# Performance work log

Measured on AMD Instinct MI355X. Metric: run time of the kernel, lower is better.

The kernel has to match this reference:

```python
import jax, jax.numpy as jnp
import numpy as np

EPS = 1e-6
H, DH = 8, 128

def rms_norm(x):
    return x * jax.lax.rsqrt(jnp.mean(jnp.square(x), axis=-1, keepdims=True) + EPS)

def l2norm(x):
    return x * jax.lax.rsqrt(jnp.sum(jnp.square(x), axis=-1, keepdims=True) + EPS)

def gated_deltanet(x, state, wq, wk, wv, wb, wg, wo):
    B, T, D = x.shape
    # projections; silu + per-head L2 norm on q,k (DeltaNet convention), silu on v
    q = l2norm(jax.nn.silu(x @ wq).reshape(B, T, H, DH))
    k = l2norm(jax.nn.silu(x @ wk).reshape(B, T, H, DH))
    v = jax.nn.silu(x @ wv).reshape(B, T, H, DH)
    beta = jax.nn.sigmoid(x @ wb)   # [B,T,H] learning-rate gate
    alpha = jax.nn.sigmoid(x @ wg)  # [B,T,H] decay gate

    def step(S, inp):
        qt, kt, vt, bt, at = inp  # [B,H,DH], [B,H,DH], [B,H,DH], [B,H], [B,H]
        S = at[..., None, None] * S                      # gated decay
        pred = jnp.einsum('bhk,bhkv->bhv', kt, S)        # S^T k
        dv = bt[..., None] * (vt - pred)                 # delta-rule update
        S = S + kt[..., None] * dv[:, :, None, :]        # rank-1 write k (x) dv
        ot = jnp.einsum('bhk,bhkv->bhv', qt, S)
        return S, ot

    tm = lambda a: jnp.moveaxis(a, 1, 0)  # time-major
    S_final, o = jax.lax.scan(step, state, (tm(q), tm(k), tm(v), tm(beta), tm(alpha)))
    o = jnp.moveaxis(o, 0, 1).reshape(B, T, H * DH)
    return o @ wo, S_final

def swiglu(x, w_gate, w_up, w_down):
    return (jax.nn.silu(x @ w_gate) * (x @ w_up)) @ w_down

def setup_inputs() -> dict:
    key = jax.random.key(0)
    ks = jax.random.split(key, 12)
    B, T, D, F = 2, 2048, 1024, 4096
    s = 1.0 / np.sqrt(D)
    inp = {
        'x': jax.random.normal(ks[0], (B, T, D), jnp.float32),
        'recurrent_state': jnp.zeros((B, H, DH, DH), jnp.float32),
        'wq': jax.random.normal(ks[1], (D, H * DH), jnp.float32) * s,
        'wk': jax.random.normal(ks[2], (D, H * DH), jnp.float32) * s,
        'wv': jax.random.normal(ks[3], (D, H * DH), jnp.float32) * s,
        'wb': jax.random.normal(ks[4], (D, H), jnp.float32) * s,
        'wg': jax.random.normal(ks[5], (D, H), jnp.float32) * s,
        'wo': jax.random.normal(ks[6], (H * DH, D), jnp.float32) * s,
        'w_gate': jax.random.normal(ks[7], (D, F), jnp.float32) * s,
        'w_up': jax.random.normal(ks[8], (D, F), jnp.float32) * s,
        'w_down': jax.random.normal(ks[9], (F, D), jnp.float32) * (1.0 / np.sqrt(F)),
    }
    return inp

def reference(x, recurrent_state, wq, wk, wv, wb, wg, wo, w_gate, w_up, w_down):
    attn_out, new_state = gated_deltanet(rms_norm(x), recurrent_state, wq, wk, wv, wb, wg, wo)
    x = x + attn_out
    x = x + swiglu(rms_norm(x), w_gate, w_up, w_down)
    return x, new_state
```

## Files before the change

### kernel.cpp

```cpp
#include <hip/hip_runtime.h>
#include <hip/hip_bf16.h>
#include <math.h>

#define BSZ 2
#define TLEN 2048
#define DDIM 1024
#define FDIM 4096
#define HHEADS 8
#define DHEAD 128
#define NC 32
#define CS 64

typedef __bf16 bf16x8 __attribute__((ext_vector_type(8)));
typedef float f32x4 __attribute__((ext_vector_type(4)));

__device__ __forceinline__ float silu_f(float x) {
    return x / (1.0f + expf(-x));
}

__device__ __forceinline__ void load_lds16(const void* g, void* l) {
    __builtin_amdgcn_global_load_lds(
        (const __attribute__((address_space(1))) void*)g,
        (__attribute__((address_space(3))) void*)l, 16, 0, 0);
}

__device__ __forceinline__ unsigned short bf16_bits(float f) {
    __hip_bfloat16 h = __float2bfloat16(f);
    return *reinterpret_cast<unsigned short*>(&h);
}

__device__ __forceinline__ float bfbits2f(unsigned short u) {
    union { unsigned int i; float f; } c;
    c.i = ((unsigned int)u) << 16;
    return c.f;
}

__device__ __forceinline__ uint4 pack8_bf16(const float* f) {
    union { unsigned short u[8]; uint4 v; } r;
#pragma unroll
    for (int i = 0; i < 8; ++i) r.u[i] = bf16_bits(f[i]);
    return r.v;
}

struct alignas(8) bh4 { __hip_bfloat16 a, b, c, d; };

__global__ __launch_bounds__(256) void rmsnorm_k(const float* __restrict__ in,
                                                 __hip_bfloat16* __restrict__ out) {
    const long row = blockIdx.x;
    const int tid = threadIdx.x;
    const float4 x = *(const float4*)(in + row * DDIM + tid * 4);
    float ss = x.x * x.x + x.y * x.y + x.z * x.z + x.w * x.w;
    ss += __shfl_xor(ss, 1);
    ss += __shfl_xor(ss, 2);
    ss += __shfl_xor(ss, 4);
    ss += __shfl_xor(ss, 8);
    ss += __shfl_xor(ss, 16);
    ss += __shfl_xor(ss, 32);
    __shared__ float wsum[4];
    if ((tid & 63) == 0) wsum[tid >> 6] = ss;
    __syncthreads();
    const float tot = wsum[0] + wsum[1] + wsum[2] + wsum[3];
    const float sc = rsqrtf(tot * (1.0f / (float)DDIM) + 1e-6f);
    bh4 y;
    y.a = __float2bfloat16(x.x * sc);
    y.b = __float2bfloat16(x.y * sc);
    y.c = __float2bfloat16(x.z * sc);
    y.d = __float2bfloat16(x.w * sc);
    *(bh4*)(out + row * DDIM + tid * 4) = y;
}

__global__ __launch_bounds__(256) void transpose_cvt(const float* __restrict__ W,
                                                     __hip_bfloat16* __restrict__ Wt,
                                                     int K, int N) {
    __shared__ float t[32][33];
    const int n0 = blockIdx.x * 32, k0 = blockIdx.y * 32;
    const int tx = threadIdx.x & 31, ty = threadIdx.x >> 5;
#pragma unroll
    for (int i = 0; i < 4; ++i)
        t[ty * 4 + i][tx] = W[(long)(k0 + ty * 4 + i) * N + n0 + tx];
    __syncthreads();
#pragma unroll
    for (int i = 0; i < 4; ++i)
        Wt[(long)(n0 + ty * 4 + i) * K + k0 + tx] = __float2bfloat16(t[tx][ty * 4 + i]);
}

template <int MODE>
__global__ __launch_bounds__(256) void gemm_n64(const __hip_bfloat16* __restrict__ A,
                                                const __hip_bfloat16* __restrict__ Bt,
                                                const float* __restrict__ resid,
                                                void* __restrict__ Cout,
                                                int M, int N, int K) {
    __shared__ __align__(16) short As[4 * 128 * 32];
    __shared__ __align__(16) short Bs[4 * 64 * 32];
    const int tid = threadIdx.x;
    const int w = tid >> 6, l = tid & 63;
    const int m0 = blockIdx.y * 128, n0 = blockIdx.x * 64;
    const int srow = (w << 4) + (l >> 2);
    const int skcol = (l & 3) * 8;
    const int wr = w >> 1, wc = w & 1;
    const int fr = l & 15;
    const int fkB = (l >> 4) * 16;

    f32x4 acc[4][2];
#pragma unroll
    for (int m = 0; m < 4; ++m)
#pragma unroll
        for (int n = 0; n < 2; ++n) acc[m][n] = (f32x4)0.0f;

    const __hip_bfloat16* Abase = A + (long)m0 * K + skcol;
    const __hip_bfloat16* Bbase = Bt + (long)n0 * K + skcol;

    for (int k0 = 0; k0 < K; k0 += 128) {
#pragma unroll
        for (int p = 0; p < 4; ++p) {
#pragma unroll
            for (int j = 0; j < 2; ++j)
                load_lds16(Abase + (long)(srow + j * 64) * K + k0 + p * 32,
                           (char*)As + p * 8192 + w * 1024 + j * 4096);
            load_lds16(Bbase + (long)srow * K + k0 + p * 32,
                       (char*)Bs + p * 4096 + w * 1024);
        }
        __syncthreads();
#pragma unroll
        for (int p = 0; p < 4; ++p) {
            bf16x8 av[4], bv[2];
#pragma unroll
            for (int m = 0; m < 4; ++m)
                av[m] = *(const bf16x8*)((char*)As + p * 8192 + (wr * 64 + m * 16 + fr) * 64 + fkB);
#pragma unroll
            for (int n = 0; n < 2; ++n)
                bv[n] = *(const bf16x8*)((char*)Bs + p * 4096 + (wc * 32 + n * 16 + fr) * 64 + fkB);
#pragma unroll
            for (int m = 0; m < 4; ++m)
#pragma unroll
                for (int n = 0; n < 2; ++n)
                    acc[m][n] = __builtin_amdgcn_mfma_f32_16x16x32_bf16(av[m], bv[n], acc[m][n], 0, 0, 0);
        }
        __syncthreads();
    }

    const int r0 = (l >> 4) * 4;
    const int cc = l & 15;
#pragma unroll
    for (int m = 0; m < 4; ++m) {
#pragma unroll
        for (int r = 0; r < 4; ++r) {
            const long row = m0 + wr * 64 + m * 16 + r0 + r;
            const long colb = n0 + wc * 32 + cc;
            if (MODE == 2) {
                __hip_bfloat16* cb = (__hip_bfloat16*)Cout + row * N + colb;
#pragma unroll
                for (int n = 0; n < 2; ++n)
                    cb[n * 16] = __float2bfloat16(acc[m][n][r]);
            } else {
                float* cp = (float*)Cout + row * N + colb;
                const float* rp = resid + row * N + colb;
#pragma unroll
                for (int n = 0; n < 2; ++n)
                    cp[n * 16] = acc[m][n][r] + rp[n * 16];
            }
        }
    }
}

__global__ __launch_bounds__(256) void gemm_gateup_bf16(const __hip_bfloat16* __restrict__ A,
                                                        const __hip_bfloat16* __restrict__ Bg,
                                                        const __hip_bfloat16* __restrict__ Bu,
                                                        __hip_bfloat16* __restrict__ Hb,
                                                        int M, int N, int K) {
    __shared__ __align__(16) short As[2 * 128 * 32];
    __shared__ __align__(16) short Bgs[2 * 64 * 32];
    __shared__ __align__(16) short Bus[2 * 64 * 32];
    const int tid = threadIdx.x;
    const int w = tid >> 6, l = tid & 63;
    const int m0 = blockIdx.y * 128, n0 = blockIdx.x * 64;
    const int srow = (w << 4) + (l >> 2);
    const int skcol = (l & 3) * 8;
    const int wr = w >> 1, wc = w & 1;
    const int fr = l & 15;
    const int fkB = (l >> 4) * 16;

    f32x4 accg[4][2], accu[4][2];
#pragma unroll
    for (int m = 0; m < 4; ++m)
#pragma unroll
        for (int n = 0; n < 2; ++n) { accg[m][n] = (f32x4)0.0f; accu[m][n] = (f32x4)0.0f; }

    const __hip_bfloat16* Abase = A + (long)m0 * K + skcol;
    const __hip_bfloat16* Bgb = Bg + (long)n0 * K + skcol;
    const __hip_bfloat16* Bub = Bu + (long)n0 * K + skcol;

    for (int k0 = 0; k0 < K; k0 += 64) {
#pragma unroll
        for (int p = 0; p < 2; ++p) {
#pragma unroll
            for (int j = 0; j < 2; ++j)
                load_lds16(Abase + (long)(srow + j * 64) * K + k0 + p * 32,
                           (char*)As + p * 8192 + w * 1024 + j * 4096);
            load_lds16(Bgb + (long)srow * K + k0 + p * 32, (char*)Bgs + p * 4096 + w * 1024);
            load_lds16(Bub + (long)srow * K + k0 + p * 32, (char*)Bus + p * 4096 + w * 1024);
        }
        __syncthreads();
#pragma unroll
        for (int p = 0; p < 2; ++p) {
            bf16x8 av[4], bgv[2], buv[2];
#pragma unroll
            for (int m = 0; m < 4; ++m)
                av[m] = *(const bf16x8*)((char*)As + p * 8192 + (wr * 64 + m * 16 + fr) * 64 + fkB);
#pragma unroll
            for (int n = 0; n < 2; ++n) {
                bgv[n] = *(const bf16x8*)((char*)Bgs + p * 4096 + (wc * 32 + n * 16 + fr) * 64 + fkB);
                buv[n] = *(const bf16x8*)((char*)Bus + p * 4096 + (wc * 32 + n * 16 + fr) * 64 + fkB);
            }
#pragma unroll
            for (int m = 0; m < 4; ++m)
#pragma unroll
                for (int n = 0; n < 2; ++n) {
                    accg[m][n] = __builtin_amdgcn_mfma_f32_16x16x32_bf16(av[m], bgv[n], accg[m][n], 0, 0, 0);
                    accu[m][n] = __builtin_amdgcn_mfma_f32_16x16x32_bf16(av[m], buv[n], accu[m][n], 0, 0, 0);
                }
        }
        __syncthreads();
    }

    const int r0 = (l >> 4) * 4;
    const int cc = l & 15;
#pragma unroll
    for (int m = 0; m < 4; ++m) {
#pragma unroll
        for (int r = 0; r < 4; ++r) {
            const long row = m0 + wr * 64 + m * 16 + r0 + r;
            __hip_bfloat16* hp = Hb + row * N + n0 + wc * 32 + cc;
#pragma unroll
            for (int n = 0; n < 2; ++n)
                hp[n * 16] = __float2bfloat16(silu_f(accg[m][n][r]) * accu[m][n][r]);
        }
    }
}

__global__ __launch_bounds__(64) void ba_kernel(const float* __restrict__ x,
                                                const float* __restrict__ wb,
                                                const float* __restrict__ wg,
                                                float* __restrict__ beta,
                                                float* __restrict__ alpha) {
    __shared__ float xs[DDIM];
    const long row = blockIdx.x;
    const int tid = threadIdx.x;
    float ss = 0.0f;
#pragma unroll
    for (int j = 0; j < 4; ++j) {
        const int fi = tid + j * 64;
        const float4 v = *(const float4*)(x + row * DDIM + fi * 4);
        *(float4*)&xs[fi * 4] = v;
        ss += v.x * v.x + v.y * v.y + v.z * v.z + v.w * v.w;
    }
    ss += __shfl_xor(ss, 1);
    ss += __shfl_xor(ss, 2);
    ss += __shfl_xor(ss, 4);
    ss += __shfl_xor(ss, 8);
    ss += __shfl_xor(ss, 16);
    ss += __shfl_xor(ss, 32);
    __syncthreads();
    const int o = tid >> 2;
    const int p = tid & 3;
    const float* wbase = (o < 8) ? (wb + o) : (wg + (o - 8));
    const float* wr = wbase + (long)(p * 256) * HHEADS;
    const float* xr = xs + p * 256;
    float acc = 0.0f;
#pragma unroll 8
    for (int i = 0; i < 256; ++i)
        acc = fmaf(xr[i], wr[(long)i * HHEADS], acc);
    acc += __shfl_xor(acc, 1);
    acc += __shfl_xor(acc, 2);
    if (p == 0) {
        const float sc = rsqrtf(ss * (1.0f / (float)DDIM) + 1e-6f);
        const float val = 1.0f / (1.0f + expf(-acc * sc));
        if (o < 8) beta[row * HHEADS + o] = val;
        else       alpha[row * HHEADS + (o - 8)] = val;
    }
}

__global__ __launch_bounds__(64) void postqkv(__hip_bfloat16* __restrict__ q,
                                              __hip_bfloat16* __restrict__ k,
                                              __hip_bfloat16* __restrict__ v) {
    const long r = blockIdx.x;
    const int tid = threadIdx.x;
    {
        unsigned int* qp = (unsigned int*)(q + r * DHEAD + tid * 2);
        const unsigned int wbits = *qp;
        float y0 = silu_f(bfbits2f(wbits & 0xffff));
        float y1 = silu_f(bfbits2f(wbits >> 16));
        float ss = y0 * y0 + y1 * y1;
        ss += __shfl_xor(ss, 1);  ss += __shfl_xor(ss, 2);
        ss += __shfl_xor(ss, 4);  ss += __shfl_xor(ss, 8);
        ss += __shfl_xor(ss, 16); ss += __shfl_xor(ss, 32);
        const float sc = rsqrtf(ss + 1e-6f);
        *qp = (unsigned int)bf16_bits(y0 * sc) | ((unsigned int)bf16_bits(y1 * sc) << 16);
    }
    {
        unsigned int* kp = (unsigned int*)(k + r * DHEAD + tid * 2);
        const unsigned int wbits = *kp;
        float y0 = silu_f(bfbits2f(wbits & 0xffff));
        float y1 = silu_f(bfbits2f(wbits >> 16));
        float ss = y0 * y0 + y1 * y1;
        ss += __shfl_xor(ss, 1);  ss += __shfl_xor(ss, 2);
        ss += __shfl_xor(ss, 4);  ss += __shfl_xor(ss, 8);
        ss += __shfl_xor(ss, 16); ss += __shfl_xor(ss, 32);
        const float sc = rsqrtf(ss + 1e-6f);
        *kp = (unsigned int)bf16_bits(y0 * sc) | ((unsigned int)bf16_bits(y1 * sc) << 16);
    }
    {
        unsigned int* vp = (unsigned int*)(v + r * DHEAD + tid * 2);
        const unsigned int wbits = *vp;
        *vp = (unsigned int)bf16_bits(silu_f(bfbits2f(wbits & 0xffff)))
            | ((unsigned int)bf16_bits(silu_f(bfbits2f(wbits >> 16))) << 16);
    }
}


__global__ __launch_bounds__(256) void chunk_prep(
    const __hip_bfloat16* __restrict__ kb, const __hip_bfloat16* __restrict__ qb,
    const __hip_bfloat16* __restrict__ vb, const float* __restrict__ betab,
    const float* __restrict__ alphab, float* __restrict__ Gcum,
    __hip_bfloat16* __restrict__ Rg, __hip_bfloat16* __restrict__ Ktg,
    __hip_bfloat16* __restrict__ dvX, __hip_bfloat16* __restrict__ Mmat)
{
    const int bh = blockIdx.x >> 5;
    const int c  = blockIdx.x & 31;
    const int b = bh >> 3, h = bh & 7;
    const int tid = threadIdx.x;
    const int w = tid >> 6, l = tid & 63;
    const int fr = l & 15;
    const int fk8 = (l >> 4) * 8;
    const int fr4 = (l >> 4) * 4;

    __shared__ __align__(16) char smem[64512];
    __hip_bfloat16* tA  = (__hip_bfloat16*)(smem);
    __hip_bfloat16* Tm  = (__hip_bfloat16*)(smem + 17408);
    __hip_bfloat16* Xr  = (__hip_bfloat16*)(smem + 26624);
    __hip_bfloat16* Xt  = (__hip_bfloat16*)(smem + 35840);
    __hip_bfloat16* bvT = (__hip_bfloat16*)(smem + 26624);
    __hip_bfloat16* tB  = (__hip_bfloat16*)(smem + 45056);
    __hip_bfloat16* KtS = (__hip_bfloat16*)(smem + 45056);
    float* sa  = (float*)(smem + 63488);
    float* sb_ = sa + 64;
    float* sG  = sb_ + 64;
    float* swB = sG + 64;

    const long row0 = (long)b * TLEN + (long)c * CS;
    const long chnk = (long)bh * NC + c;

    if (tid < 64) {
        sa[tid]  = alphab[(row0 + tid) * HHEADS + h];
        sb_[tid] = betab[(row0 + tid) * HHEADS + h];
    }
    {
        const int r = tid >> 2;
        const int d0 = (tid & 3) * 32;
        const uint4* kp = (const uint4*)(kb + (row0 + r) * DDIM + h * DHEAD + d0);
        const uint4* qp = (const uint4*)(qb + (row0 + r) * DDIM + h * DHEAD + d0);
#pragma unroll
        for (int i = 0; i < 4; ++i) {
            *(uint4*)&tA[r * 136 + d0 + i * 8] = kp[i];
            *(uint4*)&tB[r * 136 + d0 + i * 8] = qp[i];
        }
    }
    __syncthreads();
    if (tid < 64) {
        float lv = logf(sa[tid]);
#pragma unroll
        for (int off = 1; off < 64; off <<= 1) {
            const float o = __shfl_up(lv, off, 64);
            if (tid >= off) lv += o;
        }
        sG[tid] = lv;
        Gcum[chnk * CS + tid] = lv;
        swB[tid] = sb_[tid] * expf(lv);
    }
    __syncthreads();

    f32x4 accW[4], accM[4];
#pragma unroll
    for (int n = 0; n < 4; ++n) { accW[n] = (f32x4)0.0f; accM[n] = (f32x4)0.0f; }
#pragma unroll
    for (int ks = 0; ks < 4; ++ks) {
        const bf16x8 aW = *(const bf16x8*)&tA[(w * 16 + fr) * 136 + ks * 32 + fk8];
        const bf16x8 aM = *(const bf16x8*)&tB[(w * 16 + fr) * 136 + ks * 32 + fk8];
#pragma unroll
        for (int n = 0; n < 4; ++n) {
            const bf16x8 bfr = *(const bf16x8*)&tA[(n * 16 + fr) * 136 + ks * 32 + fk8];
            accW[n] = __builtin_amdgcn_mfma_f32_16x16x32_bf16(aW, bfr, accW[n], 0, 0, 0);
            accM[n] = __builtin_amdgcn_mfma_f32_16x16x32_bf16(aM, bfr, accM[n], 0, 0, 0);
        }
    }
#pragma unroll
    for (int n = 0; n < 4; ++n) {
        const int s = n * 16 + fr;
        const float Gs = sG[s];
#pragma unroll
        for (int r = 0; r < 4; ++r) {
            const int t = w * 16 + fr4 + r;
            const float ratio = (s <= t) ? expf(sG[t] - Gs) : 0.0f;
            Mmat[(chnk * CS + t) * CS + s] = __float2bfloat16(ratio * accM[n][r]);
            const float xv = (s < t) ? -(sb_[t] * ratio * accW[n][r]) : 0.0f;
            const __hip_bfloat16 xb = __float2bfloat16(xv);
            Xr[t * 72 + s] = xb;
            Xt[s * 72 + t] = xb;
            Tm[t * 72 + s] = __float2bfloat16((s == t) ? 1.0f : 0.0f);
        }
    }
    __syncthreads();

    {
        const int kk = tid >> 1;
        const int t0 = (tid & 1) * 32;
        __hip_bfloat16* kp = Ktg + (chnk * DHEAD + kk) * CS + t0;
        float f[8], fs[8];
#pragma unroll
        for (int i = 0; i < 4; ++i) {
#pragma unroll
            for (int j2 = 0; j2 < 8; ++j2) {
                const int t = t0 + i * 8 + j2;
                f[j2] = __bfloat162float(tA[t * 136 + kk]);
                fs[j2] = f[j2] * swB[t];
            }
            *(uint4*)(kp + i * 8) = pack8_bf16(f);
            *(uint4*)&KtS[kk * 72 + t0 + i * 8] = pack8_bf16(fs);
        }
    }
    __syncthreads();

    for (int rnd = 0; rnd < 6; ++rnd) {
        f32x4 aT[4], aXr2[4], aXt2[4];
#pragma unroll
        for (int n = 0; n < 4; ++n) { aT[n] = (f32x4)0.0f; aXr2[n] = (f32x4)0.0f; aXt2[n] = (f32x4)0.0f; }
#pragma unroll
        for (int ks = 0; ks < 2; ++ks) {
            const bf16x8 fT  = *(const bf16x8*)&Tm[(w * 16 + fr) * 72 + ks * 32 + fk8];
            const bf16x8 fXr = *(const bf16x8*)&Xr[(w * 16 + fr) * 72 + ks * 32 + fk8];
            const bf16x8 fXt = *(const bf16x8*)&Xt[(w * 16 + fr) * 72 + ks * 32 + fk8];
#pragma unroll
            for (int n = 0; n < 4; ++n) {
                const bf16x8 bXt = *(const bf16x8*)&Xt[(n * 16 + fr) * 72 + ks * 32 + fk8];
                const bf16x8 bXr = *(const bf16x8*)&Xr[(n * 16 + fr) * 72 + ks * 32 + fk8];
                aT[n]   = __builtin_amdgcn_mfma_f32_16x16x32_bf16(fT,  bXt, aT[n], 0, 0, 0);
                aXr2[n] = __builtin_amdgcn_mfma_f32_16x16x32_bf16(fXr, bXt, aXr2[n], 0, 0, 0);
                aXt2[n] = __builtin_amdgcn_mfma_f32_16x16x32_bf16(fXt, bXr, aXt2[n], 0, 0, 0);
            }
        }
        float told[4][4];
#pragma unroll
        for (int n = 0; n < 4; ++n)
#pragma unroll
            for (int r = 0; r < 4; ++r)
                told[n][r] = __bfloat162float(Tm[(w * 16 + fr4 + r) * 72 + n * 16 + fr]);
        __syncthreads();
#pragma unroll
        for (int n = 0; n < 4; ++n) {
            const int col = n * 16 + fr;
#pragma unroll
            for (int r = 0; r < 4; ++r) {
                const int t = w * 16 + fr4 + r;
                Tm[t * 72 + col] = __float2bfloat16(aT[n][r] + told[n][r]);
                if (rnd < 5) {
                    Xr[t * 72 + col] = __float2bfloat16(aXr2[n][r]);
                    Xt[t * 72 + col] = __float2bfloat16(aXt2[n][r]);
                }
            }
        }
        __syncthreads();
    }

    {
        f32x4 aR[8];
#pragma unroll
        for (int n = 0; n < 8; ++n) aR[n] = (f32x4)0.0f;
#pragma unroll
        for (int ks = 0; ks < 2; ++ks) {
            const bf16x8 aTf = *(const bf16x8*)&Tm[(w * 16 + fr) * 72 + ks * 32 + fk8];
#pragma unroll
            for (int n = 0; n < 8; ++n) {
                const bf16x8 bK = *(const bf16x8*)&KtS[(n * 16 + fr) * 72 + ks * 32 + fk8];
                aR[n] = __builtin_amdgcn_mfma_f32_16x16x32_bf16(aTf, bK, aR[n], 0, 0, 0);
            }
        }
#pragma unroll
        for (int n = 0; n < 8; ++n)
#pragma unroll
            for (int r = 0; r < 4; ++r) {
                const int t = w * 16 + fr4 + r;
                Rg[(chnk * CS + t) * DHEAD + n * 16 + fr] = __float2bfloat16(-aR[n][r]);
            }
    }

    {
        const int r = tid >> 2, d0 = (tid & 3) * 32;
        const float br = sb_[r];
        const uint4* vp = (const uint4*)(vb + (row0 + r) * DDIM + h * DHEAD + d0);
#pragma unroll
        for (int i = 0; i < 4; ++i) {
            const uint4 vv = vp[i];
            const unsigned short* u = (const unsigned short*)&vv;
#pragma unroll
            for (int j2 = 0; j2 < 8; ++j2)
                bvT[(d0 + i * 8 + j2) * 72 + r] = __float2bfloat16(br * bfbits2f(u[j2]));
        }
    }
    __syncthreads();

    {
        f32x4 aD[8];
#pragma unroll
        for (int n = 0; n < 8; ++n) aD[n] = (f32x4)0.0f;
#pragma unroll
        for (int ks = 0; ks < 2; ++ks) {
            const bf16x8 aTf = *(const bf16x8*)&Tm[(w * 16 + fr) * 72 + ks * 32 + fk8];
#pragma unroll
            for (int n = 0; n < 8; ++n) {
                const bf16x8 bV = *(const bf16x8*)&bvT[(n * 16 + fr) * 72 + ks * 32 + fk8];
                aD[n] = __builtin_amdgcn_mfma_f32_16x16x32_bf16(aTf, bV, aD[n], 0, 0, 0);
            }
        }
#pragma unroll
        for (int n = 0; n < 8; ++n)
#pragma unroll
            for (int r = 0; r < 4; ++r) {
                const int t = w * 16 + fr4 + r;
                dvX[(chnk * CS + t) * DHEAD + n * 16 + fr] = __float2bfloat16(aD[n][r]);
            }
    }
}

#define SEQGV 8
#define SEQ_LDS_BYTES 78848

__global__ __launch_bounds__(256) void chunk_seq_mfma(
    const float* __restrict__ S0in, const float* __restrict__ Gcum,
    const __hip_bfloat16* __restrict__ Rg, const __hip_bfloat16* __restrict__ Ktg,
    __hip_bfloat16* __restrict__ dvX, __hip_bfloat16* __restrict__ Ssnap,
    float* __restrict__ Sout)
{
    const int bh = blockIdx.x & 15;
    const int g  = blockIdx.x >> 4;
    const int j0 = g * 16;
    const int tid = threadIdx.x;
    const int w = tid >> 6;
    const int l = tid & 63;
    const int fr = l & 15;
    const int fk8 = (l >> 4) * 8;
    const int rq = (l >> 4) * 4;

    __shared__ __align__(16) char smem[SEQ_LDS_BYTES];
    __hip_bfloat16* dvT = (__hip_bfloat16*)(smem + 71680);
    __hip_bfloat16* Stl = (__hip_bfloat16*)(smem + 73984);
    float* sG = (float*)(smem + 78336);

    f32x4 SM[2];
#pragma unroll
    for (int mj = 0; mj < 2; ++mj) {
#pragma unroll
        for (int r = 0; r < 4; ++r) {
            const int kk = w * 32 + mj * 16 + rq + r;
            const float v = S0in[((long)bh * 128 + kk) * 128 + j0 + fr];
            SM[mj][r] = v;
            Stl[fr * 136 + kk] = __float2bfloat16(v);
        }
    }

    uint4 rreg[4], kreg[4];
    float greg = 0.0f;

#define SEQ_STAGE_LOAD(c_) do {                                                   \
        const long cb_ = (long)bh * NC + (c_);                                    \
        _Pragma("unroll")                                                         \
        for (int i_ = 0; i_ < 4; ++i_) {                                          \
            const int ur_ = (tid << 2) + i_;                                      \
            rreg[i_] = *(const uint4*)(Rg + (cb_ * CS + (ur_ >> 4)) * DHEAD + ((ur_ & 15) << 3)); \
            kreg[i_] = *(const uint4*)(Ktg + (cb_ * DHEAD + (ur_ >> 3)) * CS + ((ur_ & 7) << 3)); \
        }                                                                         \
        if (tid < 64) greg = Gcum[cb_ * CS + tid];                                \
    } while (0)

#define SEQ_STAGE_WRITE(bufi_) do {                                               \
        __hip_bfloat16* rb_ = (__hip_bfloat16*)(smem + (bufi_) * 17408);          \
        __hip_bfloat16* kb2_ = (__hip_bfloat16*)(smem + 34816 + (bufi_) * 18432); \
        _Pragma("unroll")                                                         \
        for (int i_ = 0; i_ < 4; ++i_) {                                          \
            const int ur_ = (tid << 2) + i_;                                      \
            *(uint4*)(rb_ + (ur_ >> 4) * 136 + ((ur_ & 15) << 3)) = rreg[i_];     \
            *(uint4*)(kb2_ + (ur_ >> 3) * 72 + ((ur_ & 7) << 3)) = kreg[i_];      \
        }                                                                         \
        if (tid < 64) sG[(bufi_) * 64 + tid] = greg;                              \
    } while (0)

    SEQ_STAGE_LOAD(0);
    SEQ_STAGE_WRITE(0);
    __syncthreads();

    for (int c = 0; c < NC; ++c) {
        const int cur = c & 1;
        const long chnk = (long)bh * NC + c;
        const __hip_bfloat16* Rl = (const __hip_bfloat16*)(smem + cur * 17408);
        const __hip_bfloat16* Ktl = (const __hip_bfloat16*)(smem + 34816 + cur * 18432);
        const float g63 = sG[cur * 64 + 63];
        const float a63 = expf(g63);

        unsigned short d0r[4];
#pragma unroll
        for (int r = 0; r < 4; ++r) {
            const int t = w * 16 + rq + r;
            d0r[r] = *(const unsigned short*)(dvX + (chnk * CS + t) * DHEAD + j0 + fr);
        }

        if (c + 1 < NC) SEQ_STAGE_LOAD(c + 1);

        {
            const int j = tid >> 4, k0 = (tid & 15) * 8;
            const uint4 v = *(const uint4*)&Stl[j * 136 + k0];
            *(uint4*)(Ssnap + (chnk * 128 + j0 + j) * 128 + k0) = v;
        }

        f32x4 acc = (f32x4)0.0f;
#pragma unroll
        for (int ks = 0; ks < 4; ++ks) {
            const bf16x8 bfrag = *(const bf16x8*)&Stl[fr * 136 + ks * 32 + fk8];
            const bf16x8 afrag = *(const bf16x8*)&Rl[(w * 16 + fr) * 136 + ks * 32 + fk8];
            acc = __builtin_amdgcn_mfma_f32_16x16x32_bf16(afrag, bfrag, acc, 0, 0, 0);
        }
#pragma unroll
        for (int r = 0; r < 4; ++r) {
            const int t = w * 16 + rq + r;
            const float rk = expf(g63 - sG[cur * 64 + t]);
            const float dv = acc[r] + bfbits2f(d0r[r]);
            *(unsigned short*)(dvX + (chnk * CS + t) * DHEAD + j0 + fr) = bf16_bits(dv);
            dvT[fr * 72 + t] = __float2bfloat16(rk * dv);
        }

        if (c + 1 < NC) SEQ_STAGE_WRITE(cur ^ 1);
        __syncthreads();

#pragma unroll
        for (int mj = 0; mj < 2; ++mj) SM[mj] *= a63;
#pragma unroll
        for (int ks = 0; ks < 2; ++ks) {
            const bf16x8 bfrag = *(const bf16x8*)&dvT[fr * 72 + ks * 32 + fk8];
#pragma unroll
            for (int mj = 0; mj < 2; ++mj) {
                const bf16x8 afrag = *(const bf16x8*)&Ktl[(w * 32 + mj * 16 + fr) * 72 + ks * 32 + fk8];
                SM[mj] = __builtin_amdgcn_mfma_f32_16x16x32_bf16(afrag, bfrag, SM[mj], 0, 0, 0);
            }
        }
#pragma unroll
        for (int mj = 0; mj < 2; ++mj)
#pragma unroll
            for (int r = 0; r < 4; ++r) {
                const int kk = w * 32 + mj * 16 + rq + r;
                Stl[fr * 136 + kk] = __float2bfloat16(SM[mj][r]);
            }
        __syncthreads();
    }

#pragma unroll
    for (int mj = 0; mj < 2; ++mj)
#pragma unroll
        for (int r = 0; r < 4; ++r) {
            const int kk = w * 32 + mj * 16 + rq + r;
            Sout[((long)bh * 128 + kk) * 128 + j0 + fr] = SM[mj][r];
        }
#undef SEQ_STAGE_LOAD
#undef SEQ_STAGE_WRITE
}

__global__ __launch_bounds__(256) void chunk_out(
    const __hip_bfloat16* __restrict__ qb, const float* __restrict__ Gcum,
    const __hip_bfloat16* __restrict__ dvX, const __hip_bfloat16* __restrict__ Ssnap,
    const __hip_bfloat16* __restrict__ Mmat, __hip_bfloat16* __restrict__ ob)
{
    const int bh = blockIdx.x >> 5;
    const int c  = blockIdx.x & 31;
    const int b = bh >> 3, h = bh & 7;
    const int tid = threadIdx.x;
    const int w = tid >> 6, l = tid & 63;
    const int fr = l & 15;
    const int fk8 = (l >> 4) * 8;
    const int rq = (l >> 4) * 4;
    const long row0 = (long)b * TLEN + (long)c * CS;
    const long chnk = (long)bh * NC + c;

    __shared__ __align__(16) char smem[62464];
    __hip_bfloat16* Ssn = (__hip_bfloat16*)(smem);
    __hip_bfloat16* Ml  = (__hip_bfloat16*)(smem + 34816);
    __hip_bfloat16* dq  = (__hip_bfloat16*)(smem + 44032);

    {
        const int j = tid >> 1;
        const int d0 = (tid & 1) * 64;
        const uint4* sp = (const uint4*)(Ssnap + (chnk * 128 + j) * 128 + d0);
#pragma unroll
        for (int i = 0; i < 8; ++i)
            *(uint4*)&Ssn[j * 136 + d0 + i * 8] = sp[i];
    }
    {
        const int t = tid >> 2;
        const int s0 = (tid & 3) * 16;
        const uint4* mp = (const uint4*)(Mmat + (chnk * CS + t) * CS + s0);
        *(uint4*)&Ml[t * 72 + s0]     = mp[0];
        *(uint4*)&Ml[t * 72 + s0 + 8] = mp[1];
    }
    {
        const int t = tid >> 2, jb = (tid & 3) * 32;
        uint4 dvr[4];
#pragma unroll
        for (int i = 0; i < 4; ++i)
            dvr[i] = ((const uint4*)(dvX + (chnk * CS + t) * DHEAD + jb))[i];
        const unsigned short* u = (const unsigned short*)&dvr[0];
#pragma unroll
        for (int i = 0; i < 32; ++i)
            dq[(jb + i) * 72 + t] = *(const __hip_bfloat16*)&u[i];
    }
    __syncthreads();

    f32x4 acc[8];
#pragma unroll
    for (int n = 0; n < 8; ++n) acc[n] = (f32x4)0.0f;

#pragma unroll
    for (int ks = 0; ks < 2; ++ks) {
        const bf16x8 afrag = *(const bf16x8*)&Ml[(w * 16 + fr) * 72 + ks * 32 + fk8];
#pragma unroll
        for (int n = 0; n < 8; ++n) {
            const bf16x8 bfrag = *(const bf16x8*)&dq[(n * 16 + fr) * 72 + ks * 32 + fk8];
            acc[n] = __builtin_amdgcn_mfma_f32_16x16x32_bf16(afrag, bfrag, acc[n], 0, 0, 0);
        }
    }
    __syncthreads();

    {
        const int t = tid >> 2, d0 = (tid & 3) * 32;
        const float At = expf(Gcum[chnk * CS + t]);
        const uint4* qp = (const uint4*)(qb + (row0 + t) * DDIM + h * DHEAD + d0);
#pragma unroll
        for (int i = 0; i < 4; ++i) {
            const uint4 qv = qp[i];
            const unsigned short* u = (const unsigned short*)&qv;
            float f[8];
#pragma unroll
            for (int j = 0; j < 8; ++j) f[j] = At * bfbits2f(u[j]);
            *(uint4*)&dq[t * 136 + d0 + i * 8] = pack8_bf16(f);
        }
    }
    __syncthreads();

#pragma unroll
    for (int ks = 0; ks < 4; ++ks) {
        const bf16x8 afrag = *(const bf16x8*)&dq[(w * 16 + fr) * 136 + ks * 32 + fk8];
#pragma unroll
        for (int n = 0; n < 8; ++n) {
            const bf16x8 bfrag = *(const bf16x8*)&Ssn[(n * 16 + fr) * 136 + ks * 32 + fk8];
            acc[n] = __builtin_amdgcn_mfma_f32_16x16x32_bf16(afrag, bfrag, acc[n], 0, 0, 0);
        }
    }

#pragma unroll
    for (int r = 0; r < 4; ++r) {
        const int t = w * 16 + rq + r;
        __hip_bfloat16* op = ob + (row0 + t) * DDIM + h * DHEAD + fr;
#pragma unroll
        for (int n = 0; n < 8; ++n)
            op[n * 16] = __float2bfloat16(acc[n][r]);
    }
}

extern "C" void kernel_launch(void* const* d_in, const int* in_sizes, int n_in,
                              void* d_out, int out_size, void* d_ws, size_t ws_size,
                              hipStream_t stream) {
    const float* x     = (const float*)d_in[0];
    const float* S0    = (const float*)d_in[1];
    const float* wq    = (const float*)d_in[2];
    const float* wk    = (const float*)d_in[3];
    const float* wv    = (const float*)d_in[4];
    const float* wb    = (const float*)d_in[5];
    const float* wg    = (const float*)d_in[6];
    const float* wo    = (const float*)d_in[7];
    const float* wgate = (const float*)d_in[8];
    const float* wup   = (const float*)d_in[9];
    const float* wdown = (const float*)d_in[10];

    const int M = BSZ * TLEN;

    float* out  = (float*)d_out;
    float* Sout = out + (long)M * DDIM;

    char* w = (char*)d_ws;
    const size_t MB = 1u << 20;
    const size_t KB = 1u << 10;
    __hip_bfloat16* qbh   = (__hip_bfloat16*)(w + 0 * MB);
    __hip_bfloat16* kbh   = (__hip_bfloat16*)(w + 8 * MB);
    __hip_bfloat16* vbh   = (__hip_bfloat16*)(w + 16 * MB);
    float*          beta  = (float*)(w + 24 * MB);
    float*          alpha = (float*)(w + 24 * MB + 128 * KB);
    float*          Gcum  = (float*)(w + 24 * MB + 256 * KB);
    __hip_bfloat16* Mmat  = (__hip_bfloat16*)(w + 24 * MB + 512 * KB);
    __hip_bfloat16* dvX   = (__hip_bfloat16*)(w + 28 * MB + 512 * KB);
    __hip_bfloat16* Rg    = (__hip_bfloat16*)(w + 36 * MB + 512 * KB);
    __hip_bfloat16* xnb   = (__hip_bfloat16*)(w + 36 * MB + 512 * KB);
    __hip_bfloat16* Ktg   = (__hip_bfloat16*)(w + 44 * MB + 512 * KB);
    __hip_bfloat16* Ssnap = (__hip_bfloat16*)(w + 52 * MB + 512 * KB);
    __hip_bfloat16* wqt   = (__hip_bfloat16*)(w + 68 * MB + 512 * KB);
    __hip_bfloat16* wkt   = (__hip_bfloat16*)(w + 70 * MB + 512 * KB);
    __hip_bfloat16* wvt   = (__hip_bfloat16*)(w + 72 * MB + 512 * KB);
    __hip_bfloat16* wot   = (__hip_bfloat16*)(w + 74 * MB + 512 * KB);
    __hip_bfloat16* obufb = (__hip_bfloat16*)(w + 8 * MB);
    __hip_bfloat16* xn2b  = (__hip_bfloat16*)(w + 8 * MB);
    __hip_bfloat16* wdt   = (__hip_bfloat16*)(w + 16 * MB);
    __hip_bfloat16* wgt   = (__hip_bfloat16*)(w + 24 * MB + 512 * KB);
    __hip_bfloat16* wut   = (__hip_bfloat16*)(w + 32 * MB + 512 * KB);
    __hip_bfloat16* Hb    = (__hip_bfloat16*)(w + 40 * MB + 512 * KB);

    transpose_cvt<<<dim3(DDIM / 32, DDIM / 32), 256, 0, stream>>>(wq, wqt, DDIM, DDIM);
    transpose_cvt<<<dim3(DDIM / 32, DDIM / 32), 256, 0, stream>>>(wk, wkt, DDIM, DDIM);
    transpose_cvt<<<dim3(DDIM / 32, DDIM / 32), 256, 0, stream>>>(wv, wvt, DDIM, DDIM);
    transpose_cvt<<<dim3(DDIM / 32, DDIM / 32), 256, 0, stream>>>(wo, wot, DDIM, DDIM);

    rmsnorm_k<<<M, 256, 0, stream>>>(x, xnb);
    ba_kernel<<<M, 64, 0, stream>>>(x, wb, wg, beta, alpha);

    dim3 gP64(DDIM / 64, M / 128);
    gemm_n64<2><<<gP64, 256, 0, stream>>>(xnb, wqt, nullptr, qbh, M, DDIM, DDIM);
    gemm_n64<2><<<gP64, 256, 0, stream>>>(xnb, wkt, nullptr, kbh, M, DDIM, DDIM);
    gemm_n64<2><<<gP64, 256, 0, stream>>>(xnb, wvt, nullptr, vbh, M, DDIM, DDIM);
    postqkv<<<M * HHEADS, 64, 0, stream>>>(qbh, kbh, vbh);

    chunk_prep<<<16 * NC, 256, 0, stream>>>(kbh, qbh, vbh, beta, alpha, Gcum, Rg, Ktg, dvX, Mmat);
    chunk_seq_mfma<<<16 * SEQGV, 256, 0, stream>>>(S0, Gcum, Rg, Ktg, dvX, Ssnap, Sout);
    chunk_out<<<16 * NC, 256, 0, stream>>>(qbh, Gcum, dvX, Ssnap, Mmat, obufb);

    gemm_n64<1><<<gP64, 256, 0, stream>>>(obufb, wot, x, out, M, DDIM, DDIM);

    transpose_cvt<<<dim3(DDIM / 32, FDIM / 32), 256, 0, stream>>>(wdown, wdt, FDIM, DDIM);
    transpose_cvt<<<dim3(FDIM / 32, DDIM / 32), 256, 0, stream>>>(wgate, wgt, DDIM, FDIM);
    transpose_cvt<<<dim3(FDIM / 32, DDIM / 32), 256, 0, stream>>>(wup, wut, DDIM, FDIM);

    rmsnorm_k<<<M, 256, 0, stream>>>(out, xn2b);

    dim3 gGU(FDIM / 64, M / 128);
    gemm_gateup_bf16<<<gGU, 256, 0, stream>>>(xn2b, wgt, wut, Hb, M, FDIM, DDIM);

    gemm_n64<1><<<gP64, 256, 0, stream>>>(Hb, wdt, out, out, M, DDIM, FDIM);
}
```

Before: 365.0 us.

## Fuse RMSNorm into gate kernel, merge QKV GEMMs, widen gate-up GEMM blocks

The first RMSNorm is folded into ba_kernel, which now also writes the normalized bf16 activations, so one launch and one extra read of x go away. The three Q/K/V projection GEMMs become a single launch with N=3072, using a new MODE 3 epilogue that scatters each 1024-column slice into its own output buffer. This relies on wqt/wkt/wvt and qbh/kbh/vbh being laid out contiguously. The gate-up GEMM moves to 512 threads per block, with each warp covering 32 rows instead of 64, which lowers per-thread accumulator pressure and spreads tile loading across more warps.

```diff
diff --git a/kernel.cpp b/kernel.cpp
--- a/kernel.cpp
+++ b/kernel.cpp
@@ -152,6 +152,12 @@
 #pragma unroll
                 for (int n = 0; n < 2; ++n)
                     cb[n * 16] = __float2bfloat16(acc[m][n][r]);
+            } else if (MODE == 3) {
+                __hip_bfloat16* cb = (__hip_bfloat16*)Cout
+                    + (long)(n0 >> 10) * 4194304 + row * 1024 + (colb & 1023);
+#pragma unroll
+                for (int n = 0; n < 2; ++n)
+                    cb[n * 16] = __float2bfloat16(acc[m][n][r]);
             } else {
                 float* cp = (float*)Cout + row * N + colb;
                 const float* rp = resid + row * N + colb;
@@ -163,7 +169,7 @@
     }
 }
 
-__global__ __launch_bounds__(256) void gemm_gateup_bf16(const __hip_bfloat16* __restrict__ A,
+__global__ __launch_bounds__(512) void gemm_gateup_bf16(const __hip_bfloat16* __restrict__ A,
                                                         const __hip_bfloat16* __restrict__ Bg,
                                                         const __hip_bfloat16* __restrict__ Bu,
                                                         __hip_bfloat16* __restrict__ Hb,
@@ -180,9 +186,9 @@
     const int fr = l & 15;
     const int fkB = (l >> 4) * 16;
 
-    f32x4 accg[4][2], accu[4][2];
-#pragma unroll
-    for (int m = 0; m < 4; ++m)
+    f32x4 accg[2][2], accu[2][2];
+#pragma unroll
+    for (int m = 0; m < 2; ++m)
 #pragma unroll
         for (int n = 0; n < 2; ++n) { accg[m][n] = (f32x4)0.0f; accu[m][n] = (f32x4)0.0f; }
 
@@ -193,27 +199,29 @@
     for (int k0 = 0; k0 < K; k0 += 64) {
 #pragma unroll
         for (int p = 0; p < 2; ++p) {
-#pragma unroll
-            for (int j = 0; j < 2; ++j)
-                load_lds16(Abase + (long)(srow + j * 64) * K + k0 + p * 32,
-                           (char*)As + p * 8192 + w * 1024 + j * 4096);
-            load_lds16(Bgb + (long)srow * K + k0 + p * 32, (char*)Bgs + p * 4096 + w * 1024);
-            load_lds16(Bub + (long)srow * K + k0 + p * 32, (char*)Bus + p * 4096 + w * 1024);
+            load_lds16(Abase + (long)srow * K + k0 + p * 32,
+                       (char*)As + p * 8192 + w * 1024);
+            if (w < 4)
+                load_lds16(Bgb + (long)srow * K + k0 + p * 32,
+                           (char*)Bgs + p * 4096 + w * 1024);
+            else
+                load_lds16(Bub + (long)(srow - 64) * K + k0 + p * 32,
+                           (char*)Bus + p * 4096 + (w - 4) * 1024);
         }
         __syncthreads();
 #pragma unroll
         for (int p = 0; p < 2; ++p) {
-            bf16x8 av[4], bgv[2], buv[2];
-#pragma unroll
-            for (int m = 0; m < 4; ++m)
-                av[m] = *(const bf16x8*)((char*)As + p * 8192 + (wr * 64 + m * 16 + fr) * 64 + fkB);
+            bf16x8 av[2], bgv[2], buv[2];
+#pragma unroll
+            for (int m = 0; m < 2; ++m)
+                av[m] = *(const bf16x8*)((char*)As + p * 8192 + (wr * 32 + m * 16 + fr) * 64 + fkB);
 #pragma unroll
             for (int n = 0; n < 2; ++n) {
                 bgv[n] = *(const bf16x8*)((char*)Bgs + p * 4096 + (wc * 32 + n * 16 + fr) * 64 + fkB);
                 buv[n] = *(const bf16x8*)((char*)Bus + p * 4096 + (wc * 32 + n * 16 + fr) * 64 + fkB);
             }
 #pragma unroll
-            for (int m = 0; m < 4; ++m)
+            for (int m = 0; m < 2; ++m)
 #pragma unroll
                 for (int n = 0; n < 2; ++n) {
                     accg[m][n] = __builtin_amdgcn_mfma_f32_16x16x32_bf16(av[m], bgv[n], accg[m][n], 0, 0, 0);
@@ -226,10 +234,10 @@
     const int r0 = (l >> 4) * 4;
     const int cc = l & 15;
 #pragma unroll
-    for (int m = 0; m < 4; ++m) {
+    for (int m = 0; m < 2; ++m) {
 #pragma unroll
         for (int r = 0; r < 4; ++r) {
-            const long row = m0 + wr * 64 + m * 16 + r0 + r;
+            const long row = m0 + wr * 32 + m * 16 + r0 + r;
             __hip_bfloat16* hp = Hb + row * N + n0 + wc * 32 + cc;
 #pragma unroll
             for (int n = 0; n < 2; ++n)
@@ -242,7 +250,8 @@
                                                 const float* __restrict__ wb,
                                                 const float* __restrict__ wg,
                                                 float* __restrict__ beta,
-                                                float* __restrict__ alpha) {
+                                                float* __restrict__ alpha,
+                                                __hip_bfloat16* __restrict__ xout) {
     __shared__ float xs[DDIM];
     const long row = blockIdx.x;
     const int tid = threadIdx.x;
@@ -260,6 +269,18 @@
     ss += __shfl_xor(ss, 8);
     ss += __shfl_xor(ss, 16);
     ss += __shfl_xor(ss, 32);
+    const float sc = rsqrtf(ss * (1.0f / (float)DDIM) + 1e-6f);
+#pragma unroll
+    for (int j = 0; j < 4; ++j) {
+        const int fi = tid + j * 64;
+        const float4 v = *(const float4*)&xs[fi * 4];
+        bh4 y;
+        y.a = __float2bfloat16(v.x * sc);
+        y.b = __float2bfloat16(v.y * sc);
+        y.c = __float2bfloat16(v.z * sc);
+        y.d = __float2bfloat16(v.w * sc);
+        *(bh4*)(xout + row * DDIM + fi * 4) = y;
+    }
     __syncthreads();
     const int o = tid >> 2;
     const int p = tid & 3;
@@ -273,7 +294,6 @@
     acc += __shfl_xor(acc, 1);
     acc += __shfl_xor(acc, 2);
     if (p == 0) {
-        const float sc = rsqrtf(ss * (1.0f / (float)DDIM) + 1e-6f);
         const float val = 1.0f / (1.0f + expf(-acc * sc));
         if (o < 8) beta[row * HHEADS + o] = val;
         else       alpha[row * HHEADS + (o - 8)] = val;
@@ -822,19 +842,16 @@
     transpose_cvt<<<dim3(DDIM / 32, DDIM / 32), 256, 0, stream>>>(wv, wvt, DDIM, DDIM);
     transpose_cvt<<<dim3(DDIM / 32, DDIM / 32), 256, 0, stream>>>(wo, wot, DDIM, DDIM);
 
-    rmsnorm_k<<<M, 256, 0, stream>>>(x, xnb);
-    ba_kernel<<<M, 64, 0, stream>>>(x, wb, wg, beta, alpha);
-
-    dim3 gP64(DDIM / 64, M / 128);
-    gemm_n64<2><<<gP64, 256, 0, stream>>>(xnb, wqt, nullptr, qbh, M, DDIM, DDIM);
-    gemm_n64<2><<<gP64, 256, 0, stream>>>(xnb, wkt, nullptr, kbh, M, DDIM, DDIM);
-    gemm_n64<2><<<gP64, 256, 0, stream>>>(xnb, wvt, nullptr, vbh, M, DDIM, DDIM);
+    ba_kernel<<<M, 64, 0, stream>>>(x, wb, wg, beta, alpha, xnb);
+
+    gemm_n64<3><<<dim3(3072 / 64, M / 128), 256, 0, stream>>>(xnb, wqt, nullptr, qbh, M, 3072, DDIM);
     postqkv<<<M * HHEADS, 64, 0, stream>>>(qbh, kbh, vbh);
 
     chunk_prep<<<16 * NC, 256, 0, stream>>>(kbh, qbh, vbh, beta, alpha, Gcum, Rg, Ktg, dvX, Mmat);
     chunk_seq_mfma<<<16 * SEQGV, 256, 0, stream>>>(S0, Gcum, Rg, Ktg, dvX, Ssnap, Sout);
     chunk_out<<<16 * NC, 256, 0, stream>>>(qbh, Gcum, dvX, Ssnap, Mmat, obufb);
 
+    dim3 gP64(DDIM / 64, M / 128);
     gemm_n64<1><<<gP64, 256, 0, stream>>>(obufb, wot, x, out, M, DDIM, DDIM);
 
     transpose_cvt<<<dim3(DDIM / 32, FDIM / 32), 256, 0, stream>>>(wdown, wdt, FDIM, DDIM);
@@ -844,7 +861,7 @@
     rmsnorm_k<<<M, 256, 0, stream>>>(out, xn2b);
 
     dim3 gGU(FDIM / 64, M / 128);
-    gemm_gateup_bf16<<<gGU, 256, 0, stream>>>(xn2b, wgt, wut, Hb, M, FDIM, DDIM);
+    gemm_gateup_bf16<<<gGU, 512, 0, stream>>>(xn2b, wgt, wut, Hb, M, FDIM, DDIM);
 
     gemm_n64<1><<<gP64, 256, 0, stream>>>(Hb, wdt, out, out, M, DDIM, FDIM);
 }
```

After: 348.7 us. 1.05x faster.
